# Performance work log

Hardware: AMD Instinct MI355X
Metric: run time of the kernel (lower is better)

The kernel has to match this reference:

```python
import jax, jax.numpy as jnp
import numpy as np

DIM = 256
HID = 1024
BATCH = 16384
STEP_SIZE = 0.1
NSTEPS = 10  # int(1.0 / step_size)


def setup_inputs() -> dict:
    key = jax.random.key(0)
    ks = jax.random.split(key, 8)
    x = jax.random.normal(ks[0], (BATCH, DIM), dtype=jnp.float32)
    # Scaled init so tanh layers stay in a sane range (like default torch init).
    W1 = jax.random.normal(ks[1], (DIM + 1, HID), dtype=jnp.float32) / np.sqrt(DIM + 1)
    b1 = jnp.zeros((HID,), dtype=jnp.float32)
    W2 = jax.random.normal(ks[2], (HID, HID), dtype=jnp.float32) / np.sqrt(HID)
    b2 = jnp.zeros((HID,), dtype=jnp.float32)
    W3 = jax.random.normal(ks[3], (HID, DIM), dtype=jnp.float32) / np.sqrt(HID)
    b3 = jnp.zeros((DIM,), dtype=jnp.float32)
    proj_mat = jax.random.normal(ks[4], (DIM, DIM), dtype=jnp.float32)
    return {"x": x, "W1": W1, "b1": b1, "W2": W2, "b2": b2,
            "W3": W3, "b3": b3, "proj_mat": proj_mat}


def reference(x, W1, b1, W2, b2, W3, b3, proj_mat):
    """FlowProposal.log_prob: backward RK4 integration of dx/dt = v(x,t)
    from t=1 to t=0 with Hutchinson trace estimation via forward-mode JVP.
    Returns log q(x), shape [batch]."""
    dtype = x.dtype

    def net(xc, t):
        # VelocityMLP: concat(x, t) -> tanh MLP -> velocity [B, DIM]
        tcol = jnp.broadcast_to(jnp.asarray(t, dtype), (xc.shape[0], 1))
        h = jnp.tanh(jnp.concatenate([xc, tcol], axis=1) @ W1 + b1)
        h = jnp.tanh(h @ W2 + b2)
        return h @ W3 + b3

    # Deterministic hashed Hutchinson noise (from the INITIAL x, as in torch).
    noise = jnp.sin((x @ proj_mat) * 1000.0) * 1.41421356  # sqrt(2)

    def dyn(xc, t):
        v, jv = jax.jvp(lambda xi: net(xi, t), (xc,), (noise,))
        tr = jnp.sum(noise * jv, axis=1, keepdims=True)  # eps^T J eps, [B,1]
        return v, tr

    dt = -STEP_SIZE

    def step(carry, k):
        xt, ljt = carry
        t = 1.0 + dt * k
        v1, tr1 = dyn(xt, t)
        v2, tr2 = dyn(xt + dt * 0.5 * v1, t + dt * 0.5)
        v3, tr3 = dyn(xt + dt * 0.5 * v2, t + dt * 0.5)
        v4, tr4 = dyn(xt + dt * v3, t + dt)
        xt = xt + (dt / 6.0) * (v1 + 2 * v2 + 2 * v3 + v4)
        ljt = ljt + (dt / 6.0) * (tr1 + 2 * tr2 + 2 * tr3 + tr4)
        return (xt, ljt), None

    init = (x, jnp.zeros((x.shape[0], 1), dtype))
    (xt, ljt), _ = jax.lax.scan(step, init, jnp.arange(NSTEPS, dtype=dtype))

    log_prob_z = -0.5 * jnp.sum(xt * xt, axis=1) - 0.5 * DIM * jnp.log(jnp.asarray(2.0 * np.pi, dtype))
    return log_prob_z - ljt[:, 0]
```

## Files before the change

### kernel.cpp

```cpp
#include <hip/hip_runtime.h>
#include <stdint.h>
#include <stddef.h>

typedef unsigned short ushort_t;
typedef float f32x4 __attribute__((ext_vector_type(4)));
typedef short short8 __attribute__((ext_vector_type(8)));

#define NB 16384
#define DIMX 256
#define HIDX 1024
#define DTC (-0.1f)

__device__ __forceinline__ unsigned short f2bf_bits(float f){
  unsigned int u = __float_as_uint(f);
  unsigned int r = (u + 0x7FFFu + ((u >> 16) & 1u)) >> 16;
  return (unsigned short)r;
}
__device__ __forceinline__ float bf2f_bits(unsigned short s){
  return __uint_as_float(((unsigned int)s) << 16);
}
__device__ __forceinline__ float fast_tanh(float x){
  float a = fabsf(x);
  float e = __expf(a + a);
  float r = 1.0f - 2.0f / (e + 1.0f);
  return copysignf(r, x);
}
__device__ __forceinline__ void gload16(const void* g, void* l){
  __builtin_amdgcn_global_load_lds(
      (const __attribute__((address_space(1))) void*)g,
      (__attribute__((address_space(3))) void*)l, 16, 0, 0);
}
template<int N> __device__ __forceinline__ void wait_vmcnt(){
  if constexpr (N == 0)      asm volatile("s_waitcnt vmcnt(0)" ::: "memory");
  else if constexpr (N == 4) asm volatile("s_waitcnt vmcnt(4)" ::: "memory");
  else if constexpr (N == 6) asm volatile("s_waitcnt vmcnt(6)" ::: "memory");
  else if constexpr (N == 8) asm volatile("s_waitcnt vmcnt(8)" ::: "memory");
  else if constexpr (N == 12) asm volatile("s_waitcnt vmcnt(12)" ::: "memory");
  else if constexpr (N == 16) asm volatile("s_waitcnt vmcnt(16)" ::: "memory");
  else static_assert(N == 0, "unsupported vmcnt");
}
__device__ __forceinline__ int ldsx(int r, int c){
  return r * 64 + (c ^ ((r & 7) << 3));
}

__global__ void prep_weights(const float* __restrict__ W1, const float* __restrict__ W2,
                             const float* __restrict__ W3,
                             ushort_t* __restrict__ W1at, ushort_t* __restrict__ W2t,
                             ushort_t* __restrict__ W3t){
  int i = blockIdx.x * blockDim.x + threadIdx.x;
  const int T1 = 1024 * 256, T2 = 1024 * 1024, T3 = 256 * 1024;
  if (i < T1){
    int n = i >> 8, k = i & 255;
    W1at[i] = f2bf_bits(W1[k * 1024 + n]);
  } else if (i < T1 + T2){
    int j = i - T1; int n = j >> 10, k = j & 1023;
    W2t[j] = f2bf_bits(W2[k * 1024 + n]);
  } else if (i < T1 + T2 + T3){
    int j = i - T1 - T2; int n = j >> 10, k = j & 1023;
    W3t[j] = f2bf_bits(W3[k * 256 + n]);
  }
}

__global__ void noise_init(const float* __restrict__ x, const float* __restrict__ proj,
                           float* __restrict__ noise_f, ushort_t* __restrict__ noise_bf,
                           float* __restrict__ xt, ushort_t* __restrict__ xcbf,
                           float* __restrict__ ljt){
  const int r0 = blockIdx.x * 8;
  const int j = threadIdx.x;
  __shared__ float xrow[8][256];
  #pragma unroll
  for (int r = 0; r < 8; ++r) xrow[r][j] = x[(size_t)(r0 + r) * 256 + j];
  __syncthreads();
  float s[8] = {0.f,0.f,0.f,0.f,0.f,0.f,0.f,0.f};
  for (int k = 0; k < 256; ++k){
    float p = proj[k * 256 + j];
    #pragma unroll
    for (int r = 0; r < 8; ++r) s[r] = fmaf(xrow[r][k], p, s[r]);
  }
  #pragma unroll
  for (int r = 0; r < 8; ++r){
    float nz = sinf(s[r] * 1000.0f) * 1.41421356237f;
    size_t idx = (size_t)(r0 + r) * 256 + j;
    noise_f[idx] = nz;
    noise_bf[idx] = f2bf_bits(nz);
    float xv = xrow[r][j];
    xt[idx] = xv;
    xcbf[idx] = f2bf_bits(xv);
  }
  if (j < 8) ljt[r0 + j] = 0.0f;
}

template<int BM, int BN, int WGM, int K, int DUAL, int EPI, int PIPE>
__launch_bounds__(512, 2)
__global__ void gemm_kernel(const ushort_t* __restrict__ A1, const ushort_t* __restrict__ A2,
                            const ushort_t* __restrict__ Wt,
                            ushort_t* __restrict__ out1, ushort_t* __restrict__ out2,
                            const float* __restrict__ bias, const float* __restrict__ w1trow,
                            float tval,
                            const ushort_t* __restrict__ dz1,
                            float* __restrict__ xt, float* __restrict__ vacc,
                            ushort_t* __restrict__ xcbf, const float* __restrict__ noise_f,
                            float* __restrict__ ljt, float wdt6, int rk){
  constexpr int BK = 64;
  constexpr int WGN = 8 / WGM;
  constexpr int WM = BM / WGM, WN = BN / WGN;
  constexpr int M_REP = WM / 16, N_REP = WN / 16;
  constexpr int ATILES = DUAL ? 2 : 1;
  constexpr int CH_A = BM / 8;
  constexpr int CH_TOT = ATILES * CH_A + BN / 8;
  constexpr int CH_PW = CH_TOT / 8;
  constexpr int BUF_E = (ATILES * BM + BN) * BK;
  constexpr int NBUF = PIPE ? 2 : 1;
  constexpr int NK = K / BK;
  static_assert(!PIPE || NK >= 2, "pipeline needs >=2 K-steps");

  __shared__ __align__(16) ushort_t lds[NBUF * BUF_E];

  const int m0 = blockIdx.x * BM;
  const int n0 = blockIdx.y * BN;
  const int tid = threadIdx.x;
  const int lane = tid & 63;
  const int wid = tid >> 6;
  const int wr = wid / WGN;
  const int wc = wid % WGN;

  f32x4 acc1[M_REP][N_REP] = {};
  f32x4 acc2[M_REP][N_REP] = {};

  const int srow = lane >> 3;
  const int scol = ((lane & 7) ^ srow) * 8;

  const ushort_t* srcb[CH_PW];
  #pragma unroll
  for (int c = 0; c < CH_PW; ++c){
    const int ch = wid * CH_PW + c;
    if (ch < CH_A)
      srcb[c] = A1 + (size_t)(m0 + ch * 8 + srow) * K + scol;
    else if (DUAL && ch < 2 * CH_A)
      srcb[c] = A2 + (size_t)(m0 + (ch - CH_A) * 8 + srow) * K + scol;
    else
      srcb[c] = Wt + (size_t)(n0 + (ch - ATILES * CH_A) * 8 + srow) * K + scol;
  }

  auto do_stage = [&](int buf, int ks){
    ushort_t* dst = lds + buf * BUF_E + (wid * CH_PW) * 512;
    const int k0 = ks * BK;
    #pragma unroll
    for (int c = 0; c < CH_PW; ++c)
      gload16(srcb[c] + k0, dst + c * 512);
  };

  auto compute = [&](int buf){
    const ushort_t* ldsA1 = lds + buf * BUF_E;
    const ushort_t* ldsA2 = ldsA1 + BM * BK;
    const ushort_t* ldsB  = ldsA1 + ATILES * BM * BK;
    #pragma unroll
    for (int kk = 0; kk < 2; ++kk){
      short8 a1f[M_REP], a2f[M_REP], bfr[N_REP];
      const int lco = kk * 32 + (lane >> 4) * 8;
      const int lro = lane & 15;
      #pragma unroll
      for (int m = 0; m < M_REP; ++m){
        int r = wr * WM + m * 16 + lro;
        a1f[m] = *(const short8*)(ldsA1 + ldsx(r, lco));
        if (DUAL) a2f[m] = *(const short8*)(ldsA2 + ldsx(r, lco));
      }
      #pragma unroll
      for (int n = 0; n < N_REP; ++n){
        int cN = wc * WN + n * 16 + lro;
        bfr[n] = *(const short8*)(ldsB + ldsx(cN, lco));
      }
      #pragma unroll
      for (int m = 0; m < M_REP; ++m){
        #pragma unroll
        for (int n = 0; n < N_REP; ++n){
          acc1[m][n] = __builtin_amdgcn_mfma_f32_16x16x32_bf16(a1f[m], bfr[n], acc1[m][n], 0, 0, 0);
          if (DUAL)
            acc2[m][n] = __builtin_amdgcn_mfma_f32_16x16x32_bf16(a2f[m], bfr[n], acc2[m][n], 0, 0, 0);
        }
      }
    }
  };

  if constexpr (PIPE){
    do_stage(0, 0);
    do_stage(1, 1);
    for (int ks = 0; ks < NK - 2; ++ks){
      wait_vmcnt<CH_PW>();
      __builtin_amdgcn_s_barrier();
      compute(ks & 1);
      asm volatile("s_waitcnt lgkmcnt(0)" ::: "memory");
      __builtin_amdgcn_s_barrier();
      do_stage(ks & 1, ks + 2);
    }
    wait_vmcnt<CH_PW>();
    __builtin_amdgcn_s_barrier();
    compute(NK & 1);
    wait_vmcnt<0>();
    __builtin_amdgcn_s_barrier();
    compute((NK - 1) & 1);
  } else {
    for (int ks = 0; ks < NK; ++ks){
      do_stage(0, ks);
      __syncthreads();
      compute(0);
      __syncthreads();
    }
  }

  const int rbase = (lane >> 4) * 4;
  const int cbase = lane & 15;
  if (EPI <= 2){
    #pragma unroll
    for (int m = 0; m < M_REP; ++m){
      #pragma unroll
      for (int n = 0; n < N_REP; ++n){
        #pragma unroll
        for (int j = 0; j < 4; ++j){
          const int R = m0 + wr * WM + m * 16 + rbase + j;
          const int C = n0 + wc * WN + n * 16 + cbase;
          const size_t idx = (size_t)R * HIDX + C;
          float a = acc1[m][n][j];
          if (EPI == 0){
            out1[idx] = f2bf_bits(a);
          } else if (EPI == 1){
            float z = a + bias[C] + tval * w1trow[C];
            float h = fast_tanh(z);
            out1[idx] = f2bf_bits(h);
            float d = bf2f_bits(dz1[idx]);
            out2[idx] = f2bf_bits((1.0f - h * h) * d);
          } else {
            float h = fast_tanh(a + bias[C]);
            out1[idx] = f2bf_bits(h);
            out2[idx] = f2bf_bits((1.0f - h * h) * acc2[m][n][j]);
          }
        }
      }
    }
  } else {
    #pragma unroll
    for (int m = 0; m < M_REP; ++m){
      #pragma unroll
      for (int j = 0; j < 4; ++j){
        const int R = m0 + wr * WM + m * 16 + rbase + j;
        float psum = 0.0f;
        #pragma unroll
        for (int n = 0; n < N_REP; ++n){
          const int C = n0 + wc * WN + n * 16 + cbase;
          const size_t idx = (size_t)R * DIMX + C;
          float v = acc1[m][n][j] + bias[C];
          float xtv = xt[idx];
          if (rk == 0){
            vacc[idx] = v;
            xcbf[idx] = f2bf_bits(xtv + 0.5f * DTC * v);
          } else if (rk == 1){
            vacc[idx] += 2.0f * v;
            xcbf[idx] = f2bf_bits(xtv + 0.5f * DTC * v);
          } else if (rk == 2){
            vacc[idx] += 2.0f * v;
            xcbf[idx] = f2bf_bits(xtv + DTC * v);
          } else {
            float xtn = xtv + (DTC / 6.0f) * (vacc[idx] + v);
            xt[idx] = xtn;
            xcbf[idx] = f2bf_bits(xtn);
          }
          psum += noise_f[idx] * acc2[m][n][j];
        }
        #pragma unroll
        for (int off = 1; off < 16; off <<= 1) psum += __shfl_xor(psum, off, 64);
        if (cbase == 0) atomicAdd(&ljt[R], wdt6 * psum);
      }
    }
  }
}

__global__ void final_kernel(const float* __restrict__ xt, const float* __restrict__ ljt,
                             float* __restrict__ out){
  const int row = blockIdx.x * 4 + (threadIdx.x >> 6);
  const int lane = threadIdx.x & 63;
  const float4 xv = *(const float4*)(xt + (size_t)row * 256 + lane * 4);
  float s = xv.x * xv.x + xv.y * xv.y + xv.z * xv.z + xv.w * xv.w;
  #pragma unroll
  for (int off = 32; off; off >>= 1) s += __shfl_xor(s, off, 64);
  if (lane == 0) out[row] = -0.5f * s - 235.2482645f - ljt[row];
}

extern "C" void kernel_launch(void* const* d_in, const int* in_sizes, int n_in,
                              void* d_out, int out_size, void* d_ws, size_t ws_size,
                              hipStream_t stream){
  (void)in_sizes; (void)n_in; (void)out_size; (void)ws_size;
  const float* x    = (const float*)d_in[0];
  const float* W1   = (const float*)d_in[1];
  const float* b1   = (const float*)d_in[2];
  const float* W2   = (const float*)d_in[3];
  const float* b2   = (const float*)d_in[4];
  const float* W3   = (const float*)d_in[5];
  const float* b3   = (const float*)d_in[6];
  const float* proj = (const float*)d_in[7];

  size_t off = 0;
  char* wsb = (char*)d_ws;
  auto carve = [&](size_t n) -> char* {
    char* p = wsb + off; off += (n + 255) & ~(size_t)255; return p;
  };
  ushort_t* W1at     = (ushort_t*)carve((size_t)1024 * 256 * 2);
  ushort_t* W2t      = (ushort_t*)carve((size_t)1024 * 1024 * 2);
  ushort_t* W3t      = (ushort_t*)carve((size_t)256 * 1024 * 2);
  float*    noise_f  = (float*)carve((size_t)NB * 256 * 4);
  ushort_t* noise_bf = (ushort_t*)carve((size_t)NB * 256 * 2);
  ushort_t* dz1      = (ushort_t*)carve((size_t)NB * 1024 * 2);
  float*    xt       = (float*)carve((size_t)NB * 256 * 4);
  ushort_t* xcbf     = (ushort_t*)carve((size_t)NB * 256 * 2);
  float*    vacc     = (float*)carve((size_t)NB * 256 * 4);
  float*    ljt      = (float*)carve((size_t)NB * 4);
  ushort_t* h1       = (ushort_t*)carve((size_t)NB * 1024 * 2);
  ushort_t* dh1      = (ushort_t*)carve((size_t)NB * 1024 * 2);
  ushort_t* h2       = (ushort_t*)carve((size_t)NB * 1024 * 2);
  ushort_t* dh2      = (ushort_t*)carve((size_t)NB * 1024 * 2);

  prep_weights<<<6144, 256, 0, stream>>>(W1, W2, W3, W1at, W2t, W3t);
  noise_init<<<NB / 8, 256, 0, stream>>>(x, proj, noise_f, noise_bf, xt, xcbf, ljt);

  gemm_kernel<256, 256, 2, 256, 0, 0, 0><<<dim3(NB / 256, 4), 512, 0, stream>>>(
      noise_bf, nullptr, W1at, dz1, nullptr, nullptr, nullptr, 0.f, nullptr,
      nullptr, nullptr, nullptr, nullptr, nullptr, 0.f, 0);

  const float toff[4] = {0.0f, -0.05f, -0.05f, -0.1f};
  const float wst[4]  = {1.0f, 2.0f, 2.0f, 1.0f};
  for (int k = 0; k < 10; ++k){
    float t = 1.0f - 0.1f * (float)k;
    for (int s = 0; s < 4; ++s){
      gemm_kernel<256, 256, 2, 256, 0, 1, 0><<<dim3(NB / 256, 4), 512, 0, stream>>>(
          xcbf, nullptr, W1at, h1, dh1, b1, W1 + 256 * 1024, t + toff[s], dz1,
          nullptr, nullptr, nullptr, nullptr, nullptr, 0.f, 0);
      gemm_kernel<128, 256, 2, 1024, 1, 2, 1><<<dim3(NB / 128, 4), 512, 0, stream>>>(
          h1, dh1, W2t, h2, dh2, b2, nullptr, 0.f, nullptr,
          nullptr, nullptr, nullptr, nullptr, nullptr, 0.f, 0);
      gemm_kernel<128, 128, 4, 1024, 1, 3, 0><<<dim3(NB / 128, 2), 512, 0, stream>>>(
          h2, dh2, W3t, nullptr, nullptr, b3, nullptr, 0.f, nullptr,
          xt, vacc, xcbf, noise_f, ljt, wst[s] * (DTC / 6.0f), s);
    }
  }
  final_kernel<<<NB / 4, 256, 0, stream>>>(xt, ljt, (float*)d_out);
}
```

Baseline: 6.677 ms.

## Fold Hutchinson trace into layer-2 epilogue via precomputed W3·noise projection

The trace eps^T J eps is rewritten as dh2 · (W3 eps), with g = noise @ W3^T precomputed once per call. The layer-3 GEMM therefore no longer needs a tangent pass and becomes single-operand. The layer-2 epilogue computes dh2 on the fly and reduces it against g into ljt, so dh2 is never written to memory. Layer 1 no longer writes dh1; instead the layer-2 kernel rebuilds the tangent operand (1-h^2)*dz1 from the h1 and dz1 tiles while loading LDS fragments. This removes the dh1/dh2 HBM traffic and half of the layer-3 MFMA work, at the cost of extra per-fragment ALU work in the layer-2 inner loop and slightly different bf16 rounding of the trace.

Measured after the change: 6.646 ms. About the same (-0.5%).

```diff
diff --git a/kernel.cpp b/kernel.cpp
--- a/kernel.cpp
+++ b/kernel.cpp
@@ -5,6 +5,7 @@
 typedef unsigned short ushort_t;
 typedef float f32x4 __attribute__((ext_vector_type(4)));
 typedef short short8 __attribute__((ext_vector_type(8)));
+typedef unsigned int u32x4 __attribute__((ext_vector_type(4)));
 
 #define NB 16384
 #define DIMX 256
@@ -42,13 +43,32 @@
 __device__ __forceinline__ int ldsx(int r, int c){
   return r * 64 + (c ^ ((r & 7) << 3));
 }
+__device__ __forceinline__ short8 tangent_frag(short8 h, short8 dz){
+  union Cv { short8 s; u32x4 u; };
+  Cv H, D, R;
+  H.s = h; D.s = dz;
+  #pragma unroll
+  for (int w = 0; w < 4; ++w){
+    unsigned hw = H.u[w], dw = D.u[w];
+    float hlo = __uint_as_float(hw << 16);
+    float hhi = __uint_as_float(hw & 0xffff0000u);
+    float dlo = __uint_as_float(dw << 16);
+    float dhi = __uint_as_float(dw & 0xffff0000u);
+    float rlo = fmaf(-hlo, hlo, 1.0f) * dlo;
+    float rhi = fmaf(-hhi, hhi, 1.0f) * dhi;
+    unsigned ulo = (__float_as_uint(rlo) + 0x8000u) >> 16;
+    unsigned uhi = (__float_as_uint(rhi) + 0x8000u) & 0xffff0000u;
+    R.u[w] = uhi | ulo;
+  }
+  return R.s;
+}
 
 __global__ void prep_weights(const float* __restrict__ W1, const float* __restrict__ W2,
                              const float* __restrict__ W3,
                              ushort_t* __restrict__ W1at, ushort_t* __restrict__ W2t,
-                             ushort_t* __restrict__ W3t){
+                             ushort_t* __restrict__ W3t, ushort_t* __restrict__ W3n){
   int i = blockIdx.x * blockDim.x + threadIdx.x;
-  const int T1 = 1024 * 256, T2 = 1024 * 1024, T3 = 256 * 1024;
+  const int T1 = 1024 * 256, T2 = 1024 * 1024, T3 = 256 * 1024, T4 = 1024 * 256;
   if (i < T1){
     int n = i >> 8, k = i & 255;
     W1at[i] = f2bf_bits(W1[k * 1024 + n]);
@@ -58,11 +78,14 @@
   } else if (i < T1 + T2 + T3){
     int j = i - T1 - T2; int n = j >> 10, k = j & 1023;
     W3t[j] = f2bf_bits(W3[k * 256 + n]);
+  } else if (i < T1 + T2 + T3 + T4){
+    int j = i - T1 - T2 - T3;
+    W3n[j] = f2bf_bits(W3[j]);
   }
 }
 
 __global__ void noise_init(const float* __restrict__ x, const float* __restrict__ proj,
-                           float* __restrict__ noise_f, ushort_t* __restrict__ noise_bf,
+                           ushort_t* __restrict__ noise_bf,
                            float* __restrict__ xt, ushort_t* __restrict__ xcbf,
                            float* __restrict__ ljt){
   const int r0 = blockIdx.x * 8;
@@ -81,7 +104,6 @@
   for (int r = 0; r < 8; ++r){
     float nz = sinf(s[r] * 1000.0f) * 1.41421356237f;
     size_t idx = (size_t)(r0 + r) * 256 + j;
-    noise_f[idx] = nz;
     noise_bf[idx] = f2bf_bits(nz);
     float xv = xrow[r][j];
     xt[idx] = xv;
@@ -94,12 +116,12 @@
 __launch_bounds__(512, 2)
 __global__ void gemm_kernel(const ushort_t* __restrict__ A1, const ushort_t* __restrict__ A2,
                             const ushort_t* __restrict__ Wt,
-                            ushort_t* __restrict__ out1, ushort_t* __restrict__ out2,
+                            ushort_t* __restrict__ out1,
                             const float* __restrict__ bias, const float* __restrict__ w1trow,
                             float tval,
-                            const ushort_t* __restrict__ dz1,
+                            const ushort_t* __restrict__ gtr,
                             float* __restrict__ xt, float* __restrict__ vacc,
-                            ushort_t* __restrict__ xcbf, const float* __restrict__ noise_f,
+                            ushort_t* __restrict__ xcbf,
                             float* __restrict__ ljt, float wdt6, int rk){
   constexpr int BK = 64;
   constexpr int WGN = 8 / WGM;
@@ -163,7 +185,10 @@
       for (int m = 0; m < M_REP; ++m){
         int r = wr * WM + m * 16 + lro;
         a1f[m] = *(const short8*)(ldsA1 + ldsx(r, lco));
-        if (DUAL) a2f[m] = *(const short8*)(ldsA2 + ldsx(r, lco));
+        if (DUAL){
+          short8 dzr = *(const short8*)(ldsA2 + ldsx(r, lco));
+          a2f[m] = tangent_frag(a1f[m], dzr);
+        }
       }
       #pragma unroll
       for (int n = 0; n < N_REP; ++n){
@@ -210,7 +235,7 @@
 
   const int rbase = (lane >> 4) * 4;
   const int cbase = lane & 15;
-  if (EPI <= 2){
+  if (EPI <= 1){
     #pragma unroll
     for (int m = 0; m < M_REP; ++m){
       #pragma unroll
@@ -223,21 +248,14 @@
           float a = acc1[m][n][j];
           if (EPI == 0){
             out1[idx] = f2bf_bits(a);
-          } else if (EPI == 1){
+          } else {
             float z = a + bias[C] + tval * w1trow[C];
-            float h = fast_tanh(z);
-            out1[idx] = f2bf_bits(h);
-            float d = bf2f_bits(dz1[idx]);
-            out2[idx] = f2bf_bits((1.0f - h * h) * d);
-          } else {
-            float h = fast_tanh(a + bias[C]);
-            out1[idx] = f2bf_bits(h);
-            out2[idx] = f2bf_bits((1.0f - h * h) * acc2[m][n][j]);
+            out1[idx] = f2bf_bits(fast_tanh(z));
           }
         }
       }
     }
-  } else {
+  } else if (EPI == 2){
     #pragma unroll
     for (int m = 0; m < M_REP; ++m){
       #pragma unroll
@@ -246,6 +264,26 @@
         float psum = 0.0f;
         #pragma unroll
         for (int n = 0; n < N_REP; ++n){
+          const int C = n0 + wc * WN + n * 16 + cbase;
+          const size_t idx = (size_t)R * HIDX + C;
+          float h = fast_tanh(acc1[m][n][j] + bias[C]);
+          out1[idx] = f2bf_bits(h);
+          float dh2 = fmaf(-h, h, 1.0f) * acc2[m][n][j];
+          psum += dh2 * bf2f_bits(gtr[idx]);
+        }
+        #pragma unroll
+        for (int off = 1; off < 16; off <<= 1) psum += __shfl_xor(psum, off, 64);
+        if (cbase == 0) atomicAdd(&ljt[R], wdt6 * psum);
+      }
+    }
+  } else {
+    #pragma unroll
+    for (int m = 0; m < M_REP; ++m){
+      #pragma unroll
+      for (int n = 0; n < N_REP; ++n){
+        #pragma unroll
+        for (int j = 0; j < 4; ++j){
+          const int R = m0 + wr * WM + m * 16 + rbase + j;
           const int C = n0 + wc * WN + n * 16 + cbase;
           const size_t idx = (size_t)R * DIMX + C;
           float v = acc1[m][n][j] + bias[C];
@@ -264,11 +302,7 @@
             xt[idx] = xtn;
             xcbf[idx] = f2bf_bits(xtn);
           }
-          psum += noise_f[idx] * acc2[m][n][j];
-        }
-        #pragma unroll
-        for (int off = 1; off < 16; off <<= 1) psum += __shfl_xor(psum, off, 64);
-        if (cbase == 0) atomicAdd(&ljt[R], wdt6 * psum);
+        }
       }
     }
   }
@@ -306,24 +340,26 @@
   ushort_t* W1at     = (ushort_t*)carve((size_t)1024 * 256 * 2);
   ushort_t* W2t      = (ushort_t*)carve((size_t)1024 * 1024 * 2);
   ushort_t* W3t      = (ushort_t*)carve((size_t)256 * 1024 * 2);
-  float*    noise_f  = (float*)carve((size_t)NB * 256 * 4);
+  ushort_t* W3n      = (ushort_t*)carve((size_t)1024 * 256 * 2);
   ushort_t* noise_bf = (ushort_t*)carve((size_t)NB * 256 * 2);
   ushort_t* dz1      = (ushort_t*)carve((size_t)NB * 1024 * 2);
+  ushort_t* gtr      = (ushort_t*)carve((size_t)NB * 1024 * 2);
   float*    xt       = (float*)carve((size_t)NB * 256 * 4);
   ushort_t* xcbf     = (ushort_t*)carve((size_t)NB * 256 * 2);
   float*    vacc     = (float*)carve((size_t)NB * 256 * 4);
   float*    ljt      = (float*)carve((size_t)NB * 4);
   ushort_t* h1       = (ushort_t*)carve((size_t)NB * 1024 * 2);
-  ushort_t* dh1      = (ushort_t*)carve((size_t)NB * 1024 * 2);
   ushort_t* h2       = (ushort_t*)carve((size_t)NB * 1024 * 2);
-  ushort_t* dh2      = (ushort_t*)carve((size_t)NB * 1024 * 2);
-
-  prep_weights<<<6144, 256, 0, stream>>>(W1, W2, W3, W1at, W2t, W3t);
-  noise_init<<<NB / 8, 256, 0, stream>>>(x, proj, noise_f, noise_bf, xt, xcbf, ljt);
+
+  prep_weights<<<7168, 256, 0, stream>>>(W1, W2, W3, W1at, W2t, W3t, W3n);
+  noise_init<<<NB / 8, 256, 0, stream>>>(x, proj, noise_bf, xt, xcbf, ljt);
 
   gemm_kernel<256, 256, 2, 256, 0, 0, 0><<<dim3(NB / 256, 4), 512, 0, stream>>>(
-      noise_bf, nullptr, W1at, dz1, nullptr, nullptr, nullptr, 0.f, nullptr,
-      nullptr, nullptr, nullptr, nullptr, nullptr, 0.f, 0);
+      noise_bf, nullptr, W1at, dz1, nullptr, nullptr, 0.f, nullptr,
+      nullptr, nullptr, nullptr, nullptr, 0.f, 0);
+  gemm_kernel<256, 256, 2, 256, 0, 0, 0><<<dim3(NB / 256, 4), 512, 0, stream>>>(
+      noise_bf, nullptr, W3n, gtr, nullptr, nullptr, 0.f, nullptr,
+      nullptr, nullptr, nullptr, nullptr, 0.f, 0);
 
   const float toff[4] = {0.0f, -0.05f, -0.05f, -0.1f};
   const float wst[4]  = {1.0f, 2.0f, 2.0f, 1.0f};
@@ -331,14 +367,14 @@
     float t = 1.0f - 0.1f * (float)k;
     for (int s = 0; s < 4; ++s){
       gemm_kernel<256, 256, 2, 256, 0, 1, 0><<<dim3(NB / 256, 4), 512, 0, stream>>>(
-          xcbf, nullptr, W1at, h1, dh1, b1, W1 + 256 * 1024, t + toff[s], dz1,
-          nullptr, nullptr, nullptr, nullptr, nullptr, 0.f, 0);
-      gemm_kernel<128, 256, 2, 1024, 1, 2, 1><<<dim3(NB / 128, 4), 512, 0, stream>>>(
-          h1, dh1, W2t, h2, dh2, b2, nullptr, 0.f, nullptr,
-          nullptr, nullptr, nullptr, nullptr, nullptr, 0.f, 0);
-      gemm_kernel<128, 128, 4, 1024, 1, 3, 0><<<dim3(NB / 128, 2), 512, 0, stream>>>(
-          h2, dh2, W3t, nullptr, nullptr, b3, nullptr, 0.f, nullptr,
-          xt, vacc, xcbf, noise_f, ljt, wst[s] * (DTC / 6.0f), s);
+          xcbf, nullptr, W1at, h1, b1, W1 + 256 * 1024, t + toff[s], nullptr,
+          nullptr, nullptr, nullptr, nullptr, 0.f, 0);
+      gemm_kernel<128, 256, 2, 1024, 2, 2, 1><<<dim3(NB / 128, 4), 512, 0, stream>>>(
+          h1, dz1, W2t, h2, b2, nullptr, 0.f, gtr,
+          nullptr, nullptr, nullptr, ljt, wst[s] * (DTC / 6.0f), 0);
+      gemm_kernel<128, 128, 4, 1024, 0, 3, 0><<<dim3(NB / 128, 2), 512, 0, stream>>>(
+          h2, nullptr, W3t, nullptr, b3, nullptr, 0.f, nullptr,
+          xt, vacc, xcbf, nullptr, 0.f, s);
     }
   }
   final_kernel<<<NB / 4, 256, 0, stream>>>(xt, ljt, (float*)d_out);
```
